# Kernel tuning notes

Hardware: AMD Instinct MI355X
Metric: run time of the kernel (lower is better)

## Reference

```python
import jax, jax.numpy as jnp
import numpy as np

N, C, E, H, K, GH, L = 50000, 256, 800000, 64, 32, 64, 2
EPS = 1e-8
LN_EPS = 1e-5


def setup_inputs() -> dict:
    key = jax.random.key(0)
    ks = jax.random.split(key, 24)
    s = lambda fan_in: 1.0 / np.sqrt(fan_in)
    inp = {
        "x": jax.random.normal(ks[0], (N, C), jnp.float32),
        "src": jax.random.randint(ks[1], (E,), 0, N),
        "dst": jax.random.randint(ks[2], (E,), 0, N),
        "base_w": jax.random.uniform(ks[3], (E,), jnp.float32),
        # encoder: Linear(C,H) -> ReLU -> Linear(H,H) -> ReLU  (weights stored [in,out])
        "enc_w1": jax.random.normal(ks[4], (C, H), jnp.float32) * s(C),
        "enc_b1": jnp.zeros((H,), jnp.float32),
        "enc_w2": jax.random.normal(ks[5], (H, H), jnp.float32) * s(H),
        "enc_b2": jnp.zeros((H,), jnp.float32),
        # edge gate: Linear(2H, GH) -> ReLU -> Linear(GH, 1) -> sigmoid
        "gate_w1": jax.random.normal(ks[6], (2 * H, GH), jnp.float32) * s(2 * H),
        "gate_b1": jnp.zeros((GH,), jnp.float32),
        "gate_w2": jax.random.normal(ks[7], (GH, 1), jnp.float32) * 0.1,
        "gate_b2": jnp.full((1,), 2.0, jnp.float32),
        # per-layer update MLPs (stacked over L layers): Linear(H,H)->ReLU->Linear(H,H)
        "upd_w1": jax.random.normal(ks[8], (L, H, H), jnp.float32) * s(H),
        "upd_b1": jnp.zeros((L, H), jnp.float32),
        "upd_w2": jax.random.normal(ks[9], (L, H, H), jnp.float32) * s(H),
        "upd_b2": jnp.zeros((L, H), jnp.float32),
        # per-layer LayerNorm params
        "ln_g": jnp.ones((L, H), jnp.float32),
        "ln_b": jnp.zeros((L, H), jnp.float32),
        # node reliability logits
        "rho_raw": jax.random.normal(ks[10], (N,), jnp.float32) * 0.1,
        # toU head: Linear(H, K)
        "toU_w": jax.random.normal(ks[11], (H, K), jnp.float32) * 0.1,
        "toU_b": jnp.ones((K,), jnp.float32),
    }
    return inp


def reference(x, src, dst, base_w,
              enc_w1, enc_b1, enc_w2, enc_b2,
              gate_w1, gate_b1, gate_w2, gate_b2,
              upd_w1, upd_b1, upd_w2, upd_b2,
              ln_g, ln_b, rho_raw, toU_w, toU_b):
    relu = jax.nn.relu
    # node encoder
    h = relu(relu(x @ enc_w1 + enc_b1) @ enc_w2 + enc_b2)  # [N, H]
    rho = jax.nn.sigmoid(rho_raw)                          # [N]
    rho_e = rho[src] * rho[dst]                            # [E]
    for l in range(L):
        h_src = h[src]                                     # [E, H] gather
        h_dst = h[dst]                                     # [E, H] gather
        z = relu(jnp.concatenate([h_src, h_dst], axis=1) @ gate_w1 + gate_b1)
        gate = jax.nn.sigmoid((z @ gate_w2 + gate_b2)[:, 0])  # [E]
        w = base_w * gate * rho_e                           # [E]
        # weighted scatter-add aggregate with degree normalization
        m = jax.ops.segment_sum(w[:, None] * h_src, dst, num_segments=N)  # [N, H]
        deg = jax.ops.segment_sum(w, dst, num_segments=N)                 # [N]
        neigh = m / (deg[:, None] + EPS)
        u = relu(neigh @ upd_w1[l] + upd_b1[l]) @ upd_w2[l] + upd_b2[l]
        pre = h + u
        mean = jnp.mean(pre, axis=-1, keepdims=True)
        var = jnp.var(pre, axis=-1, keepdims=True)
        h = (pre - mean) / jnp.sqrt(var + LN_EPS) * ln_g[l] + ln_b[l]
    U = jax.nn.softplus(h @ toU_w + toU_b)                 # [N, K]
    return U
```

## Files before the change

### kernel.cpp

```cpp
#include <hip/hip_runtime.h>
#include <math.h>


typedef unsigned short ushort_t;
typedef __attribute__((ext_vector_type(8))) short bf16x8;
typedef __attribute__((ext_vector_type(4))) float f32x4;

__device__ __forceinline__ float bf2f(ushort_t u) {
    return __uint_as_float(((unsigned int)u) << 16);
}
__device__ __forceinline__ ushort_t f2bf(float f) {
    unsigned int x = __float_as_uint(f);
    unsigned int lsb = (x >> 16) & 1u;
    x += 0x7fffu + lsb;
    return (ushort_t)(x >> 16);
}

__global__ __launch_bounds__(256) void pack_kernel(
    const float* __restrict__ w1, const float* __restrict__ w2,
    const float* __restrict__ gw1, const float* __restrict__ uw1,
    const float* __restrict__ uw2, const float* __restrict__ tw,
    ushort_t* __restrict__ w1f, ushort_t* __restrict__ w2f,
    ushort_t* __restrict__ g1f, ushort_t* __restrict__ u1f,
    ushort_t* __restrict__ u2f, ushort_t* __restrict__ tuf) {
    int t = blockIdx.x * 256 + threadIdx.x;
    if (t < 16384) {
        int i = t & 7, l = (t >> 3) & 63, kb = (t >> 9) & 7, nt = t >> 12;
        int k = kb * 32 + (l >> 4) * 8 + i, n = nt * 16 + (l & 15);
        w1f[t] = f2bf(w1[(size_t)k * 64 + n]);
    }
    if (t < 4096) {
        int i = t & 7, l = (t >> 3) & 63, kb = (t >> 9) & 1, nt = t >> 10;
        int k = kb * 32 + (l >> 4) * 8 + i, n = nt * 16 + (l & 15);
        w2f[t] = f2bf(w2[(size_t)k * 64 + n]);
    }
    if (t < 8192) {
        int i = t & 7, l = (t >> 3) & 63, kb = (t >> 9) & 1, j = t >> 10;
        int part = j >> 2, nt = j & 3;
        int k = part * 64 + kb * 32 + (l >> 4) * 8 + i, n = nt * 16 + (l & 15);
        g1f[t] = f2bf(gw1[(size_t)k * 64 + n]);
    }
    if (t < 8192) {
        int i = t & 7, l = (t >> 3) & 63, kb = (t >> 9) & 1;
        int nt = (t >> 10) & 3, lay = t >> 12;
        int k = kb * 32 + (l >> 4) * 8 + i, n = nt * 16 + (l & 15);
        u1f[t] = f2bf(uw1[(size_t)lay * 4096 + (size_t)k * 64 + n]);
        u2f[t] = f2bf(uw2[(size_t)lay * 4096 + (size_t)k * 64 + n]);
    }
    if (t < 2048) {
        int i = t & 7, l = (t >> 3) & 63, kb = (t >> 9) & 1, nt = t >> 10;
        int k = kb * 32 + (l >> 4) * 8 + i, n = nt * 16 + (l & 15);
        tuf[t] = f2bf(tw[(size_t)k * 32 + n]);
    }
}

__global__ __launch_bounds__(256) void enc_kernel(
    const float* __restrict__ x, const ushort_t* __restrict__ w1f,
    const float* __restrict__ b1, const ushort_t* __restrict__ w2f,
    const float* __restrict__ b2, const ushort_t* __restrict__ g1f,
    const float* __restrict__ gb1,
    float* __restrict__ h, ushort_t* __restrict__ ahb,
    float* __restrict__ bbuf, int N) {
    __shared__ ushort_t xls[4][16][264];
    __shared__ ushort_t tls[4][16][72];
    const int tid  = threadIdx.x;
    const int lane = tid & 63;
    const int w    = tid >> 6;
    const int m    = lane & 15;
    const int g    = lane >> 4;
    const int rbase = blockIdx.x * 64;
    for (int p = tid; p < 64 * 64; p += 256) {
        int row = p >> 6, k4 = p & 63;
        int grow = rbase + row;
        float4 v = (grow < N) ? *(const float4*)(x + (size_t)grow * 256 + k4 * 4)
                              : make_float4(0.f, 0.f, 0.f, 0.f);
        unsigned int p0 = (unsigned int)f2bf(v.x) | ((unsigned int)f2bf(v.y) << 16);
        unsigned int p1 = (unsigned int)f2bf(v.z) | ((unsigned int)f2bf(v.w) << 16);
        *(uint2*)&xls[row >> 4][row & 15][k4 * 4] = make_uint2(p0, p1);
    }
    __syncthreads();
    f32x4 acc[4] = {{0,0,0,0},{0,0,0,0},{0,0,0,0},{0,0,0,0}};
    #pragma unroll
    for (int kb = 0; kb < 8; ++kb) {
        bf16x8 a = *(const bf16x8*)&xls[w][m][kb * 32 + g * 8];
        #pragma unroll
        for (int nt = 0; nt < 4; ++nt) {
            bf16x8 b = *(const bf16x8*)(w1f + (((size_t)nt * 8 + kb) * 64 + lane) * 8);
            acc[nt] = __builtin_amdgcn_mfma_f32_16x16x32_bf16(a, b, acc[nt], 0, 0, 0);
        }
    }
    #pragma unroll
    for (int nt = 0; nt < 4; ++nt) {
        float bb1 = b1[nt * 16 + m];
        #pragma unroll
        for (int r = 0; r < 4; ++r) {
            float tv = fmaxf(acc[nt][r] + bb1, 0.f);
            tls[w][g * 4 + r][nt * 16 + m] = f2bf(tv);
        }
    }
    f32x4 acc2[4] = {{0,0,0,0},{0,0,0,0},{0,0,0,0},{0,0,0,0}};
    #pragma unroll
    for (int kb = 0; kb < 2; ++kb) {
        bf16x8 a2 = *(const bf16x8*)&tls[w][m][kb * 32 + g * 8];
        #pragma unroll
        for (int nt = 0; nt < 4; ++nt) {
            bf16x8 b = *(const bf16x8*)(w2f + (((size_t)nt * 2 + kb) * 64 + lane) * 8);
            acc2[nt] = __builtin_amdgcn_mfma_f32_16x16x32_bf16(a2, b, acc2[nt], 0, 0, 0);
        }
    }
    #pragma unroll
    for (int nt = 0; nt < 4; ++nt) {
        float bb2 = b2[nt * 16 + m];
        #pragma unroll
        for (int r = 0; r < 4; ++r) {
            float hv = fmaxf(acc2[nt][r] + bb2, 0.f);
            int grow = rbase + w * 16 + g * 4 + r;
            ushort_t hb = f2bf(hv);
            tls[w][g * 4 + r][nt * 16 + m] = hb;
            if (grow < N) {
                h[(size_t)grow * 64 + nt * 16 + m] = hv;
                ahb[(size_t)grow * 128 + 64 + nt * 16 + m] = hb;
            }
        }
    }
    f32x4 accp[8] = {{0,0,0,0},{0,0,0,0},{0,0,0,0},{0,0,0,0},
                     {0,0,0,0},{0,0,0,0},{0,0,0,0},{0,0,0,0}};
    #pragma unroll
    for (int kb = 0; kb < 2; ++kb) {
        bf16x8 a3 = *(const bf16x8*)&tls[w][m][kb * 32 + g * 8];
        #pragma unroll
        for (int j = 0; j < 8; ++j) {
            bf16x8 b = *(const bf16x8*)(g1f + (((size_t)j * 2 + kb) * 64 + lane) * 8);
            accp[j] = __builtin_amdgcn_mfma_f32_16x16x32_bf16(a3, b, accp[j], 0, 0, 0);
        }
    }
    #pragma unroll
    for (int nt = 0; nt < 4; ++nt) {
        float gbl = gb1[nt * 16 + m];
        #pragma unroll
        for (int r = 0; r < 4; ++r) {
            int grow = rbase + w * 16 + g * 4 + r;
            if (grow < N) {
                ahb[(size_t)grow * 128 + nt * 16 + m] = f2bf(accp[nt][r] + gbl);
                bbuf[(size_t)grow * 64 + nt * 16 + m] = accp[nt + 4][r];
            }
        }
    }
}

__global__ __launch_bounds__(256) void hist_kernel(
    const int* __restrict__ dst, int* __restrict__ cnt,
    int* __restrict__ rank, int E) {
    for (int e = blockIdx.x * blockDim.x + threadIdx.x; e < E;
         e += gridDim.x * blockDim.x)
        rank[e] = atomicAdd(&cnt[dst[e]], 1);
}

__global__ __launch_bounds__(256) void scan1_kernel(
    const int* __restrict__ cnt, int* __restrict__ bsum, int N) {
    __shared__ int red[256];
    int i = blockIdx.x * 256 + threadIdx.x;
    red[threadIdx.x] = (i < N) ? cnt[i] : 0;
    __syncthreads();
    for (int off = 128; off > 0; off >>= 1) {
        if (threadIdx.x < off) red[threadIdx.x] += red[threadIdx.x + off];
        __syncthreads();
    }
    if (threadIdx.x == 0) bsum[blockIdx.x] = red[0];
}

__global__ __launch_bounds__(1024) void scan2_kernel(
    int* __restrict__ bsum, int nb) {
    __shared__ int s[1024];
    int v = (threadIdx.x < nb) ? bsum[threadIdx.x] : 0;
    s[threadIdx.x] = v;
    __syncthreads();
    for (int off = 1; off < 1024; off <<= 1) {
        int t = (threadIdx.x >= off) ? s[threadIdx.x - off] : 0;
        __syncthreads();
        s[threadIdx.x] += t;
        __syncthreads();
    }
    if (threadIdx.x < nb) bsum[threadIdx.x] = s[threadIdx.x] - v;
}

__global__ __launch_bounds__(256) void scan3_kernel(
    const int* __restrict__ cnt, const int* __restrict__ bsum,
    int* __restrict__ row_ptr, int N) {
    __shared__ int s[256];
    int i = blockIdx.x * 256 + threadIdx.x;
    int v = (i < N) ? cnt[i] : 0;
    s[threadIdx.x] = v;
    __syncthreads();
    for (int off = 1; off < 256; off <<= 1) {
        int t = (threadIdx.x >= off) ? s[threadIdx.x - off] : 0;
        __syncthreads();
        s[threadIdx.x] += t;
        __syncthreads();
    }
    if (i < N) row_ptr[i] = bsum[blockIdx.x] + s[threadIdx.x] - v;
    if (i == N - 1) row_ptr[N] = bsum[blockIdx.x] + s[threadIdx.x];
}

__global__ __launch_bounds__(256) void scatter_kernel(
    const int* __restrict__ src, const int* __restrict__ dst,
    const float* __restrict__ base_w, const float* __restrict__ rr,
    const int* __restrict__ row_ptr, const int* __restrict__ rank,
    int2* __restrict__ recs, int E) {
    for (int e = blockIdx.x * blockDim.x + threadIdx.x; e < E;
         e += gridDim.x * blockDim.x) {
        int s = src[e], d = dst[e];
        int pos = row_ptr[d] + rank[e];
        float rs = 1.f / (1.f + __expf(-rr[s]));
        float rd = 1.f / (1.f + __expf(-rr[d]));
        float c = base_w[e] * rs * rd;
        recs[pos] = make_int2(s, __float_as_int(c));
    }
}

__global__ __launch_bounds__(256) void gateagg_kernel(
    const int* __restrict__ row_ptr, const int2* __restrict__ recs,
    const ushort_t* __restrict__ ahb, const float* __restrict__ bb,
    const float* __restrict__ gw2, const float* __restrict__ gb2,
    float* __restrict__ m, float* __restrict__ deg, int N) {
    const int lane = threadIdx.x & 63;
    const int sub  = lane & 15;
    const int grp  = lane >> 4;
    const float4 gv = ((const float4*)gw2)[sub];
    const float gb = gb2[0];
    const int wid  = blockIdx.x * (blockDim.x >> 6) + (threadIdx.x >> 6);
    const int nw   = gridDim.x * (blockDim.x >> 6);
    for (int n = wid; n < N; n += nw) {
        const int beg = row_ptr[n], end = row_ptr[n + 1];
        const float4 bv = *(const float4*)(bb + (size_t)n * 64 + sub * 4);
        float m0 = 0.f, m1 = 0.f, m2 = 0.f, m3 = 0.f, dacc = 0.f;
        int i = beg + grp;
        for (; i + 4 < end; i += 8) {
            int2 rA = recs[i];
            int2 rB = recs[i + 4];
            const ushort_t* rowA = ahb + (size_t)rA.x * 128;
            const ushort_t* rowB = ahb + (size_t)rB.x * 128;
            ushort4 avA = *(const ushort4*)(rowA + sub * 4);
            ushort4 hvA = *(const ushort4*)(rowA + 64 + sub * 4);
            ushort4 avB = *(const ushort4*)(rowB + sub * 4);
            ushort4 hvB = *(const ushort4*)(rowB + 64 + sub * 4);
            float tA = fmaxf(bf2f(avA.x) + bv.x, 0.f) * gv.x
                     + fmaxf(bf2f(avA.y) + bv.y, 0.f) * gv.y
                     + fmaxf(bf2f(avA.z) + bv.z, 0.f) * gv.z
                     + fmaxf(bf2f(avA.w) + bv.w, 0.f) * gv.w;
            float tB = fmaxf(bf2f(avB.x) + bv.x, 0.f) * gv.x
                     + fmaxf(bf2f(avB.y) + bv.y, 0.f) * gv.y
                     + fmaxf(bf2f(avB.z) + bv.z, 0.f) * gv.z
                     + fmaxf(bf2f(avB.w) + bv.w, 0.f) * gv.w;
            #pragma unroll
            for (int o = 8; o > 0; o >>= 1) {
                tA += __shfl_xor(tA, o, 64);
                tB += __shfl_xor(tB, o, 64);
            }
            float wA = __int_as_float(rA.y) / (1.f + __expf(-(tA + gb)));
            float wB = __int_as_float(rB.y) / (1.f + __expf(-(tB + gb)));
            m0 = fmaf(wA, bf2f(hvA.x), m0); m0 = fmaf(wB, bf2f(hvB.x), m0);
            m1 = fmaf(wA, bf2f(hvA.y), m1); m1 = fmaf(wB, bf2f(hvB.y), m1);
            m2 = fmaf(wA, bf2f(hvA.z), m2); m2 = fmaf(wB, bf2f(hvB.z), m2);
            m3 = fmaf(wA, bf2f(hvA.w), m3); m3 = fmaf(wB, bf2f(hvB.w), m3);
            dacc += wA + wB;
        }
        if (i < end) {
            int2 r = recs[i];
            const ushort_t* row = ahb + (size_t)r.x * 128;
            ushort4 av = *(const ushort4*)(row + sub * 4);
            ushort4 hv = *(const ushort4*)(row + 64 + sub * 4);
            float t = fmaxf(bf2f(av.x) + bv.x, 0.f) * gv.x
                    + fmaxf(bf2f(av.y) + bv.y, 0.f) * gv.y
                    + fmaxf(bf2f(av.z) + bv.z, 0.f) * gv.z
                    + fmaxf(bf2f(av.w) + bv.w, 0.f) * gv.w;
            #pragma unroll
            for (int o = 8; o > 0; o >>= 1) t += __shfl_xor(t, o, 64);
            float w = __int_as_float(r.y) / (1.f + __expf(-(t + gb)));
            m0 = fmaf(w, bf2f(hv.x), m0);
            m1 = fmaf(w, bf2f(hv.y), m1);
            m2 = fmaf(w, bf2f(hv.z), m2);
            m3 = fmaf(w, bf2f(hv.w), m3);
            dacc += w;
        }
        #pragma unroll
        for (int o = 16; o < 64; o <<= 1) {
            m0 += __shfl_xor(m0, o, 64);
            m1 += __shfl_xor(m1, o, 64);
            m2 += __shfl_xor(m2, o, 64);
            m3 += __shfl_xor(m3, o, 64);
            dacc += __shfl_xor(dacc, o, 64);
        }
        if (lane < 16) {
            *(float4*)(m + (size_t)n * 64 + sub * 4) = make_float4(m0, m1, m2, m3);
            if (lane == 0) deg[n] = dacc;
        }
    }
}

template <int MODE>
__global__ __launch_bounds__(256) void upd_kernel(
    const float* __restrict__ m, const float* __restrict__ deg,
    const float* __restrict__ h_in,
    const ushort_t* __restrict__ u1f, const float* __restrict__ b1,
    const ushort_t* __restrict__ u2f, const float* __restrict__ b2,
    const float* __restrict__ lng, const float* __restrict__ lnb,
    const ushort_t* __restrict__ g1f, const float* __restrict__ gb1,
    ushort_t* __restrict__ ahb, float* __restrict__ bbuf,
    const ushort_t* __restrict__ tuf, const float* __restrict__ tub,
    float* __restrict__ h_out, float* __restrict__ U, int N) {
    __shared__ ushort_t mls[4][16][72];
    __shared__ ushort_t tls[4][16][72];
    const int tid  = threadIdx.x;
    const int lane = tid & 63;
    const int w    = tid >> 6;
    const int m_   = lane & 15;
    const int g    = lane >> 4;
    const int rbase = blockIdx.x * 64;
    for (int p = tid; p < 64 * 32; p += 256) {
        int row = p >> 5, c2 = p & 31;
        int grow = rbase + row;
        float2 v = make_float2(0.f, 0.f);
        if (grow < N) {
            float dg = deg[grow] + 1e-8f;
            float2 mv = *(const float2*)(m + (size_t)grow * 64 + c2 * 2);
            v = make_float2(mv.x / dg, mv.y / dg);
        }
        unsigned int pk = (unsigned int)f2bf(v.x) | ((unsigned int)f2bf(v.y) << 16);
        *(unsigned int*)&mls[row >> 4][row & 15][c2 * 2] = pk;
    }
    __syncthreads();
    f32x4 acc[4] = {{0,0,0,0},{0,0,0,0},{0,0,0,0},{0,0,0,0}};
    #pragma unroll
    for (int kb = 0; kb < 2; ++kb) {
        bf16x8 a = *(const bf16x8*)&mls[w][m_][kb * 32 + g * 8];
        #pragma unroll
        for (int nt = 0; nt < 4; ++nt) {
            bf16x8 b = *(const bf16x8*)(u1f + (((size_t)nt * 2 + kb) * 64 + lane) * 8);
            acc[nt] = __builtin_amdgcn_mfma_f32_16x16x32_bf16(a, b, acc[nt], 0, 0, 0);
        }
    }
    #pragma unroll
    for (int nt = 0; nt < 4; ++nt) {
        float bb1 = b1[nt * 16 + m_];
        #pragma unroll
        for (int r = 0; r < 4; ++r)
            tls[w][g * 4 + r][nt * 16 + m_] = f2bf(fmaxf(acc[nt][r] + bb1, 0.f));
    }
    f32x4 acc2[4] = {{0,0,0,0},{0,0,0,0},{0,0,0,0},{0,0,0,0}};
    #pragma unroll
    for (int kb = 0; kb < 2; ++kb) {
        bf16x8 a2 = *(const bf16x8*)&tls[w][m_][kb * 32 + g * 8];
        #pragma unroll
        for (int nt = 0; nt < 4; ++nt) {
            bf16x8 b = *(const bf16x8*)(u2f + (((size_t)nt * 2 + kb) * 64 + lane) * 8);
            acc2[nt] = __builtin_amdgcn_mfma_f32_16x16x32_bf16(a2, b, acc2[nt], 0, 0, 0);
        }
    }
    float hn_reg[4][4];
    #pragma unroll
    for (int r = 0; r < 4; ++r) {
        const int grow = rbase + w * 16 + g * 4 + r;
        float pre[4];
        float s1 = 0.f, s2 = 0.f;
        #pragma unroll
        for (int nt = 0; nt < 4; ++nt) {
            float hv = (grow < N) ? h_in[(size_t)grow * 64 + nt * 16 + m_] : 0.f;
            pre[nt] = acc2[nt][r] + b2[nt * 16 + m_] + hv;
            s1 += pre[nt];
            s2 += pre[nt] * pre[nt];
        }
        #pragma unroll
        for (int o = 1; o < 16; o <<= 1) {
            s1 += __shfl_xor(s1, o, 64);
            s2 += __shfl_xor(s2, o, 64);
        }
        float mean = s1 * (1.0f / 64.0f);
        float var  = s2 * (1.0f / 64.0f) - mean * mean;
        float rinv = rsqrtf(var + 1e-5f);
        #pragma unroll
        for (int nt = 0; nt < 4; ++nt) {
            float hn = (pre[nt] - mean) * rinv * lng[nt * 16 + m_] + lnb[nt * 16 + m_];
            hn_reg[r][nt] = hn;
            tls[w][g * 4 + r][nt * 16 + m_] = f2bf(hn);
        }
    }
    if (MODE == 0) {
        #pragma unroll
        for (int nt = 0; nt < 4; ++nt) {
            #pragma unroll
            for (int r = 0; r < 4; ++r) {
                int grow = rbase + w * 16 + g * 4 + r;
                if (grow < N) {
                    h_out[(size_t)grow * 64 + nt * 16 + m_] = hn_reg[r][nt];
                    ahb[(size_t)grow * 128 + 64 + nt * 16 + m_] = f2bf(hn_reg[r][nt]);
                }
            }
        }
        f32x4 accp[8] = {{0,0,0,0},{0,0,0,0},{0,0,0,0},{0,0,0,0},
                         {0,0,0,0},{0,0,0,0},{0,0,0,0},{0,0,0,0}};
        #pragma unroll
        for (int kb = 0; kb < 2; ++kb) {
            bf16x8 a3 = *(const bf16x8*)&tls[w][m_][kb * 32 + g * 8];
            #pragma unroll
            for (int j = 0; j < 8; ++j) {
                bf16x8 b = *(const bf16x8*)(g1f + (((size_t)j * 2 + kb) * 64 + lane) * 8);
                accp[j] = __builtin_amdgcn_mfma_f32_16x16x32_bf16(a3, b, accp[j], 0, 0, 0);
            }
        }
        #pragma unroll
        for (int nt = 0; nt < 4; ++nt) {
            float gbl = gb1[nt * 16 + m_];
            #pragma unroll
            for (int r = 0; r < 4; ++r) {
                int grow = rbase + w * 16 + g * 4 + r;
                if (grow < N) {
                    ahb[(size_t)grow * 128 + nt * 16 + m_] = f2bf(accp[nt][r] + gbl);
                    bbuf[(size_t)grow * 64 + nt * 16 + m_] = accp[nt + 4][r];
                }
            }
        }
    } else {
        f32x4 accu[2] = {{0,0,0,0},{0,0,0,0}};
        #pragma unroll
        for (int kb = 0; kb < 2; ++kb) {
            bf16x8 a3 = *(const bf16x8*)&tls[w][m_][kb * 32 + g * 8];
            #pragma unroll
            for (int nt = 0; nt < 2; ++nt) {
                bf16x8 b = *(const bf16x8*)(tuf + (((size_t)nt * 2 + kb) * 64 + lane) * 8);
                accu[nt] = __builtin_amdgcn_mfma_f32_16x16x32_bf16(a3, b, accu[nt], 0, 0, 0);
            }
        }
        #pragma unroll
        for (int nt = 0; nt < 2; ++nt) {
            float tb = tub[nt * 16 + m_];
            #pragma unroll
            for (int r = 0; r < 4; ++r) {
                int grow = rbase + w * 16 + g * 4 + r;
                if (grow < N) {
                    float av = accu[nt][r] + tb;
                    float sp = av > 0.f ? av + log1pf(__expf(-av))
                                        : log1pf(__expf(av));
                    U[(size_t)grow * 32 + nt * 16 + m_] = sp;
                }
            }
        }
    }
}

extern "C" void kernel_launch(void* const* d_in, const int* in_sizes, int n_in,
                              void* d_out, int out_size, void* d_ws, size_t ws_size,
                              hipStream_t stream) {
    const float* x       = (const float*)d_in[0];
    const int*   src     = (const int*)d_in[1];
    const int*   dst     = (const int*)d_in[2];
    const float* base_w  = (const float*)d_in[3];
    const float* enc_w1  = (const float*)d_in[4];
    const float* enc_b1  = (const float*)d_in[5];
    const float* enc_w2  = (const float*)d_in[6];
    const float* enc_b2  = (const float*)d_in[7];
    const float* gate_w1 = (const float*)d_in[8];
    const float* gate_b1 = (const float*)d_in[9];
    const float* gate_w2 = (const float*)d_in[10];
    const float* gate_b2 = (const float*)d_in[11];
    const float* upd_w1  = (const float*)d_in[12];
    const float* upd_b1  = (const float*)d_in[13];
    const float* upd_w2  = (const float*)d_in[14];
    const float* upd_b2  = (const float*)d_in[15];
    const float* ln_g    = (const float*)d_in[16];
    const float* ln_b    = (const float*)d_in[17];
    const float* rho_raw = (const float*)d_in[18];
    const float* toU_w   = (const float*)d_in[19];
    const float* toU_b   = (const float*)d_in[20];

    const int N = in_sizes[18];
    const int E = in_sizes[1];
    const int nsb = (N + 255) / 256;

    float* ws  = (float*)d_ws;
    size_t off = 0;
    float* h0  = ws + off; off += (size_t)N * 64;
    float* h1  = ws + off; off += (size_t)N * 64;
    ushort_t* ahb = (ushort_t*)(ws + off); off += (size_t)N * 64;
    float* bb  = ws + off; off += (size_t)N * 64;
    float* m   = ws + off; off += (size_t)N * 64;
    float* deg = ws + off; off += (size_t)((N + 3) & ~3);
    int* row_ptr = (int*)(ws + off); off += (size_t)((N + 1 + 3) & ~3);
    int* cnt     = (int*)(ws + off); off += (size_t)((N + 3) & ~3);
    int* bsum    = (int*)(ws + off); off += (size_t)((nsb + 3) & ~3);
    int* rank    = (int*)(ws + off); off += (size_t)E;
    int2* recs   = (int2*)(ws + off); off += (size_t)E * 2;
    ushort_t* w1f = (ushort_t*)(ws + off); off += 8192;
    ushort_t* w2f = (ushort_t*)(ws + off); off += 2048;
    ushort_t* g1f = (ushort_t*)(ws + off); off += 4096;
    ushort_t* u1f = (ushort_t*)(ws + off); off += 4096;
    ushort_t* u2f = (ushort_t*)(ws + off); off += 4096;
    ushort_t* tuf = (ushort_t*)(ws + off); off += 1024;

    pack_kernel<<<64, 256, 0, stream>>>(enc_w1, enc_w2, gate_w1, upd_w1, upd_w2,
                                        toU_w, w1f, w2f, g1f, u1f, u2f, tuf);
    const int nblk64 = (N + 63) / 64;
    enc_kernel<<<nblk64, 256, 0, stream>>>(x, w1f, enc_b1, w2f, enc_b2,
                                           g1f, gate_b1, h0, ahb, bb, N);

    hipMemsetAsync(cnt, 0, (size_t)N * sizeof(int), stream);
    hist_kernel<<<(E + 255) / 256, 256, 0, stream>>>(dst, cnt, rank, E);
    scan1_kernel<<<nsb, 256, 0, stream>>>(cnt, bsum, N);
    scan2_kernel<<<1, 1024, 0, stream>>>(bsum, nsb);
    scan3_kernel<<<nsb, 256, 0, stream>>>(cnt, bsum, row_ptr, N);
    scatter_kernel<<<(E + 255) / 256, 256, 0, stream>>>(src, dst, base_w, rho_raw,
                                                        row_ptr, rank, recs, E);

    gateagg_kernel<<<2048, 256, 0, stream>>>(row_ptr, recs, ahb, bb,
                                             gate_w2, gate_b2, m, deg, N);
    upd_kernel<0><<<nblk64, 256, 0, stream>>>(
        m, deg, h0, u1f, upd_b1, u2f, upd_b2, ln_g, ln_b,
        g1f, gate_b1, ahb, bb, tuf, toU_b, h1, (float*)d_out, N);

    gateagg_kernel<<<2048, 256, 0, stream>>>(row_ptr, recs, ahb, bb,
                                             gate_w2, gate_b2, m, deg, N);
    upd_kernel<1><<<nblk64, 256, 0, stream>>>(
        m, deg, h1, u1f + 4096, upd_b1 + 64, u2f + 4096, upd_b2 + 64,
        ln_g + 64, ln_b + 64,
        g1f, gate_b1, ahb, bb, tuf, toU_b, nullptr, (float*)d_out, N);
}
```

Baseline: 212.2 us.

## Drop fp32 h buffers, emit bf16 normalized aggregate from gateagg

Removes the fp32 copies of the node features h (h0/h1) and reads the residual from the existing bf16 feature buffer instead. The gate/aggregate kernel now divides by degree itself and writes a bf16 neighbor buffer, replacing the fp32 message and degree arrays. The update kernel loads its MFMA A operand directly from global memory rather than staging it through shared memory with a barrier. This cuts global write and read traffic between kernels, at the cost of bf16 rounding on the residual path and on the normalized aggregate.

```diff
diff --git a/kernel.cpp b/kernel.cpp
--- a/kernel.cpp
+++ b/kernel.cpp
@@ -59,8 +59,7 @@
     const float* __restrict__ b1, const ushort_t* __restrict__ w2f,
     const float* __restrict__ b2, const ushort_t* __restrict__ g1f,
     const float* __restrict__ gb1,
-    float* __restrict__ h, ushort_t* __restrict__ ahb,
-    float* __restrict__ bbuf, int N) {
+    ushort_t* __restrict__ ahb, float* __restrict__ bbuf, int N) {
     __shared__ ushort_t xls[4][16][264];
     __shared__ ushort_t tls[4][16][72];
     const int tid  = threadIdx.x;
@@ -117,10 +116,8 @@
             int grow = rbase + w * 16 + g * 4 + r;
             ushort_t hb = f2bf(hv);
             tls[w][g * 4 + r][nt * 16 + m] = hb;
-            if (grow < N) {
-                h[(size_t)grow * 64 + nt * 16 + m] = hv;
+            if (grow < N)
                 ahb[(size_t)grow * 128 + 64 + nt * 16 + m] = hb;
-            }
         }
     }
     f32x4 accp[8] = {{0,0,0,0},{0,0,0,0},{0,0,0,0},{0,0,0,0},
@@ -222,7 +219,7 @@
     const int* __restrict__ row_ptr, const int2* __restrict__ recs,
     const ushort_t* __restrict__ ahb, const float* __restrict__ bb,
     const float* __restrict__ gw2, const float* __restrict__ gb2,
-    float* __restrict__ m, float* __restrict__ deg, int N) {
+    ushort_t* __restrict__ nb, int N) {
     const int lane = threadIdx.x & 63;
     const int sub  = lane & 15;
     const int grp  = lane >> 4;
@@ -292,24 +289,27 @@
             dacc += __shfl_xor(dacc, o, 64);
         }
         if (lane < 16) {
-            *(float4*)(m + (size_t)n * 64 + sub * 4) = make_float4(m0, m1, m2, m3);
-            if (lane == 0) deg[n] = dacc;
+            float dg = dacc + 1e-8f;
+            ushort4 o4;
+            o4.x = f2bf(m0 / dg);
+            o4.y = f2bf(m1 / dg);
+            o4.z = f2bf(m2 / dg);
+            o4.w = f2bf(m3 / dg);
+            *(ushort4*)(nb + (size_t)n * 64 + sub * 4) = o4;
         }
     }
 }
 
 template <int MODE>
 __global__ __launch_bounds__(256) void upd_kernel(
-    const float* __restrict__ m, const float* __restrict__ deg,
-    const float* __restrict__ h_in,
+    const ushort_t* __restrict__ nb,
     const ushort_t* __restrict__ u1f, const float* __restrict__ b1,
     const ushort_t* __restrict__ u2f, const float* __restrict__ b2,
     const float* __restrict__ lng, const float* __restrict__ lnb,
     const ushort_t* __restrict__ g1f, const float* __restrict__ gb1,
     ushort_t* __restrict__ ahb, float* __restrict__ bbuf,
     const ushort_t* __restrict__ tuf, const float* __restrict__ tub,
-    float* __restrict__ h_out, float* __restrict__ U, int N) {
-    __shared__ ushort_t mls[4][16][72];
+    float* __restrict__ U, int N) {
     __shared__ ushort_t tls[4][16][72];
     const int tid  = threadIdx.x;
     const int lane = tid & 63;
@@ -317,23 +317,13 @@
     const int m_   = lane & 15;
     const int g    = lane >> 4;
     const int rbase = blockIdx.x * 64;
-    for (int p = tid; p < 64 * 32; p += 256) {
-        int row = p >> 5, c2 = p & 31;
-        int grow = rbase + row;
-        float2 v = make_float2(0.f, 0.f);
-        if (grow < N) {
-            float dg = deg[grow] + 1e-8f;
-            float2 mv = *(const float2*)(m + (size_t)grow * 64 + c2 * 2);
-            v = make_float2(mv.x / dg, mv.y / dg);
-        }
-        unsigned int pk = (unsigned int)f2bf(v.x) | ((unsigned int)f2bf(v.y) << 16);
-        *(unsigned int*)&mls[row >> 4][row & 15][c2 * 2] = pk;
-    }
-    __syncthreads();
+    const int arow = rbase + w * 16 + m_;
+    const bool rowok = arow < N;
     f32x4 acc[4] = {{0,0,0,0},{0,0,0,0},{0,0,0,0},{0,0,0,0}};
     #pragma unroll
     for (int kb = 0; kb < 2; ++kb) {
-        bf16x8 a = *(const bf16x8*)&mls[w][m_][kb * 32 + g * 8];
+        bf16x8 a = {0, 0, 0, 0, 0, 0, 0, 0};
+        if (rowok) a = *(const bf16x8*)(nb + (size_t)arow * 64 + kb * 32 + g * 8);
         #pragma unroll
         for (int nt = 0; nt < 4; ++nt) {
             bf16x8 b = *(const bf16x8*)(u1f + (((size_t)nt * 2 + kb) * 64 + lane) * 8);
@@ -365,7 +355,8 @@
         float s1 = 0.f, s2 = 0.f;
         #pragma unroll
         for (int nt = 0; nt < 4; ++nt) {
-            float hv = (grow < N) ? h_in[(size_t)grow * 64 + nt * 16 + m_] : 0.f;
+            float hv = (grow < N)
+                ? bf2f(ahb[(size_t)grow * 128 + 64 + nt * 16 + m_]) : 0.f;
             pre[nt] = acc2[nt][r] + b2[nt * 16 + m_] + hv;
             s1 += pre[nt];
             s2 += pre[nt] * pre[nt];
@@ -391,10 +382,8 @@
             #pragma unroll
             for (int r = 0; r < 4; ++r) {
                 int grow = rbase + w * 16 + g * 4 + r;
-                if (grow < N) {
-                    h_out[(size_t)grow * 64 + nt * 16 + m_] = hn_reg[r][nt];
+                if (grow < N)
                     ahb[(size_t)grow * 128 + 64 + nt * 16 + m_] = f2bf(hn_reg[r][nt]);
-                }
             }
         }
         f32x4 accp[8] = {{0,0,0,0},{0,0,0,0},{0,0,0,0},{0,0,0,0},
@@ -479,12 +468,9 @@
 
     float* ws  = (float*)d_ws;
     size_t off = 0;
-    float* h0  = ws + off; off += (size_t)N * 64;
-    float* h1  = ws + off; off += (size_t)N * 64;
     ushort_t* ahb = (ushort_t*)(ws + off); off += (size_t)N * 64;
     float* bb  = ws + off; off += (size_t)N * 64;
-    float* m   = ws + off; off += (size_t)N * 64;
-    float* deg = ws + off; off += (size_t)((N + 3) & ~3);
+    ushort_t* nb = (ushort_t*)(ws + off); off += (size_t)N * 32;
     int* row_ptr = (int*)(ws + off); off += (size_t)((N + 1 + 3) & ~3);
     int* cnt     = (int*)(ws + off); off += (size_t)((N + 3) & ~3);
     int* bsum    = (int*)(ws + off); off += (size_t)((nsb + 3) & ~3);
@@ -501,7 +487,7 @@
                                         toU_w, w1f, w2f, g1f, u1f, u2f, tuf);
     const int nblk64 = (N + 63) / 64;
     enc_kernel<<<nblk64, 256, 0, stream>>>(x, w1f, enc_b1, w2f, enc_b2,
-                                           g1f, gate_b1, h0, ahb, bb, N);
+                                           g1f, gate_b1, ahb, bb, N);
 
     hipMemsetAsync(cnt, 0, (size_t)N * sizeof(int), stream);
     hist_kernel<<<(E + 255) / 256, 256, 0, stream>>>(dst, cnt, rank, E);
@@ -512,15 +498,15 @@
                                                         row_ptr, rank, recs, E);
 
     gateagg_kernel<<<2048, 256, 0, stream>>>(row_ptr, recs, ahb, bb,
-                                             gate_w2, gate_b2, m, deg, N);
+                                             gate_w2, gate_b2, nb, N);
     upd_kernel<0><<<nblk64, 256, 0, stream>>>(
-        m, deg, h0, u1f, upd_b1, u2f, upd_b2, ln_g, ln_b,
-        g1f, gate_b1, ahb, bb, tuf, toU_b, h1, (float*)d_out, N);
+        nb, u1f, upd_b1, u2f, upd_b2, ln_g, ln_b,
+        g1f, gate_b1, ahb, bb, tuf, toU_b, (float*)d_out, N);
 
     gateagg_kernel<<<2048, 256, 0, stream>>>(row_ptr, recs, ahb, bb,
-                                             gate_w2, gate_b2, m, deg, N);
+                                             gate_w2, gate_b2, nb, N);
     upd_kernel<1><<<nblk64, 256, 0, stream>>>(
-        m, deg, h1, u1f + 4096, upd_b1 + 64, u2f + 4096, upd_b2 + 64,
+        nb, u1f + 4096, upd_b1 + 64, u2f + 4096, upd_b2 + 64,
         ln_g + 64, ln_b + 64,
-        g1f, gate_b1, ahb, bb, tuf, toU_b, nullptr, (float*)d_out, N);
-}
+        g1f, gate_b1, ahb, bb, tuf, toU_b, (float*)d_out, N);
+}
```

New measurement: 213.3 us. About the same (+0.5%).
